# Kernel optimization log

Hardware: AMD Instinct MI355X
Metric: run time of the kernel (lower is better)

Reference implementation:

```python
import jax, jax.numpy as jnp
import numpy as np

B, D, H = 4096, 64, 1024  # batch, state dim, hidden width


def setup_inputs() -> dict:
    key = jax.random.key(0)
    ks = jax.random.split(key, 4)
    def w(k, shape, fan_in):
        return (jax.random.normal(k, shape, jnp.float32) / np.float32(np.sqrt(fan_in)))
    return {
        "x": jax.random.normal(ks[0], (B, 1 + D), jnp.float32),
        "W1": w(ks[1], (D, H), D),
        "b1": jnp.zeros((H,), jnp.float32),
        "W2": w(ks[2], (H, H), H),
        "b2": jnp.zeros((H,), jnp.float32),
        "W3": w(ks[3], (H, D), H),
        "b3": jnp.zeros((D,), jnp.float32),
    }


def _mlp(z, W1, b1, W2, b2, W3, b3):
    # tanh MLP vector field: d -> h -> h -> d
    h = jnp.tanh(z @ W1 + b1)
    h = jnp.tanh(h @ W2 + b2)
    return h @ W3 + b3


def reference(x, W1, b1, W2, b2, W3, b3):
    x_in = x[:, 1:]                        # [B, D] state (col 0 is logp channel)
    f = lambda z: _mlp(z, W1, b1, W2, b2, W3, b3)
    x_out = f(x_in)                        # [B, D]

    # Exact Jacobian trace: same math as the torch per-dim autograd.grad loop,
    # expressed as D forward-mode JVPs vmapped over the identity basis.
    eye = jnp.eye(x_in.shape[1], dtype=x.dtype)

    def diag_entry(e):                     # e: [D] basis vector
        _, t = jax.jvp(f, (x_in,), (jnp.broadcast_to(e, x_in.shape),))
        return t @ e                       # [B] = J[:, i, i]

    trJ = jnp.sum(jax.vmap(diag_entry)(eye), axis=0)  # [B]

    out = jnp.concatenate([-trJ[:, None], x_out], axis=1)  # [B, 1+D]
    return out + 0.0 * x  # faithful to `+ 0 * x` in the original
```

## Files before the change

kernel.cpp:

```cpp
#include <hip/hip_runtime.h>
#include <cmath>

typedef unsigned short u16;
typedef __attribute__((ext_vector_type(8))) short s8v;
typedef __attribute__((ext_vector_type(4))) float f4v;
typedef __attribute__((ext_vector_type(16))) float f16v;

__device__ __forceinline__ u16 f2bf(float f) {
    union { float f; unsigned u; } v; v.f = f;
    unsigned r = v.u + 0x7FFFu + ((v.u >> 16) & 1u);
    return (u16)(r >> 16);
}
__device__ __forceinline__ float tanh_fast(float x) {
    float e = __builtin_amdgcn_exp2f(x * 2.88539008177792681f);
    return 1.f - 2.f * __builtin_amdgcn_rcpf(1.f + e);
}
__device__ __forceinline__ int wslot(int row, int c) {
    return ((((c >> 2) << 6) | ((c & 3) << 4) | (row & 15)) ^ c);
}
__device__ __forceinline__ size_t fragoff(int n, int k) {
    return (((size_t)(n >> 5) * 64 + (k >> 4)) * 64 + (n & 31) + (((k >> 3) & 1) << 5)) * 8 + (k & 7);
}
__device__ __forceinline__ void gload_lds16(const u16* g, u16* l) {
    __builtin_amdgcn_global_load_lds(
        (const __attribute__((address_space(1))) void*)g,
        (__attribute__((address_space(3))) void*)l,
        16, 0, 0);
}

__launch_bounds__(256)
__global__ void cnf_prep(const float* __restrict__ x, const float* __restrict__ W1,
                         const float* __restrict__ W2, const float* __restrict__ W3,
                         u16* __restrict__ W2Tf, u16* __restrict__ VTf,
                         u16* __restrict__ xb, u16* __restrict__ W1T,
                         u16* __restrict__ W3Tf, float* __restrict__ trJ)
{
    __shared__ float w2s[32][33];
    __shared__ __align__(16) float w1s[64][36];
    const int a = blockIdx.x * 32;
    const int b = blockIdx.y * 32;
    const int t = threadIdx.x;

    #pragma unroll
    for (int it = 0; it < 4; ++it) {
        int idx = t + it * 256;
        w2s[idx >> 5][idx & 31] = W2[(a + (idx >> 5)) * 1024 + b + (idx & 31)];
    }
    #pragma unroll
    for (int it = 0; it < 8; ++it) {
        int idx = t + it * 256;
        w1s[idx >> 5][idx & 31] = W1[(idx >> 5) * 1024 + a + (idx & 31)];
    }
    __syncthreads();

    #pragma unroll
    for (int it = 0; it < 4; ++it) {
        int idx = t + it * 256;
        int rr = idx >> 5, cc = idx & 31;
        W2Tf[fragoff(b + rr, a + cc)] = f2bf(w2s[cc][rr]);
    }
    {
        const int q = t >> 3, pg = t & 7;
        const float* w3row = W3 + (b + q) * 64;
        f4v u = f4v{0.f, 0.f, 0.f, 0.f};
        #pragma unroll
        for (int i4 = 0; i4 < 16; ++i4) {
            f4v w3v = *(const f4v*)&w3row[i4 * 4];
            #pragma unroll
            for (int s = 0; s < 4; ++s) {
                f4v wv = *(const f4v*)&w1s[i4 * 4 + s][pg * 4];
                u += w3v[s] * wv;
            }
        }
        #pragma unroll
        for (int j = 0; j < 4; ++j) {
            const int pp = pg * 4 + j;
            VTf[fragoff(b + q, a + pp)] = f2bf(w2s[pp][q] * u[j]);
        }
    }
    {
        int bid = blockIdx.y * 32 + blockIdx.x;
        int e = bid * 256 + t;
        xb[e] = f2bf(x[(e >> 6) * 65 + 1 + (e & 63)]);
    }
    if (blockIdx.y == 0) {
        int pp = t >> 3, i0 = (t & 7) * 8;
        s8v v;
        #pragma unroll
        for (int j = 0; j < 8; ++j) v[j] = (short)f2bf(w1s[i0 + j][pp]);
        *(s8v*)&W1T[(a + pp) * 64 + i0] = v;
        if (t < 128) trJ[blockIdx.x * 128 + t] = 0.f;
    }
    if (blockIdx.y == 1) {
        int idx = blockIdx.x * 256 + t;
        int n = idx & 63, k0 = (idx >> 6) * 8;
        s8v v;
        #pragma unroll
        for (int j = 0; j < 8; ++j) v[j] = (short)f2bf(W3[(k0 + j) * 64 + n]);
        *(s8v*)&W3Tf[fragoff(n, k0)] = v;
    }
}

__launch_bounds__(256)
__global__ void cnf_gemm1(const u16* __restrict__ xb, const u16* __restrict__ W1T,
                          const float* __restrict__ b1,
                          u16* __restrict__ h1f, u16* __restrict__ g1f)
{
    __shared__ __align__(16) u16 lds[12 * 1024];
    __shared__ __align__(16) u16 hls[128 * 64];
    __shared__ __align__(16) u16 gls[128 * 64];
    const int t = threadIdx.x;
    const int wave = t >> 6, lane = t & 63;
    const int wm = wave >> 1, wn = wave & 1;
    const int g = lane >> 4, lr = lane & 15;
    const int arow0 = blockIdx.x * 128, bcol0 = blockIdx.y * 64;

    #pragma unroll
    for (int i = 0; i < 4; ++i) {
        int ch = t + i * 256, row = ch >> 3, c = ch & 7;
        *(s8v*)&lds[(row >> 4) * 1024 + wslot(row, c) * 8] =
            *(const s8v*)&xb[(arow0 + row) * 64 + c * 8];
    }
    #pragma unroll
    for (int i = 0; i < 2; ++i) {
        int ch = t + i * 256, row = ch >> 3, c = ch & 7;
        *(s8v*)&lds[(8 + (row >> 4)) * 1024 + wslot(row, c) * 8] =
            *(const s8v*)&W1T[(bcol0 + row) * 64 + c * 8];
    }
    __syncthreads();

    f4v acc[4][2];
    #pragma unroll
    for (int mi = 0; mi < 4; ++mi)
        #pragma unroll
        for (int ni = 0; ni < 2; ++ni) acc[mi][ni] = f4v{0.f,0.f,0.f,0.f};

    #pragma unroll
    for (int ks = 0; ks < 2; ++ks) {
        const int lo = (ks * 64 + (lane ^ ((ks * 4 + g) & 7))) * 8;
        s8v af[4], bf[2];
        #pragma unroll
        for (int mi = 0; mi < 4; ++mi) af[mi] = *(const s8v*)&lds[(wm * 4 + mi) * 1024 + lo];
        #pragma unroll
        for (int ni = 0; ni < 2; ++ni) bf[ni] = *(const s8v*)&lds[(8 + wn * 2 + ni) * 1024 + lo];
        #pragma unroll
        for (int mi = 0; mi < 4; ++mi)
            #pragma unroll
            for (int ni = 0; ni < 2; ++ni)
                acc[mi][ni] = __builtin_amdgcn_mfma_f32_16x16x32_bf16(af[mi], bf[ni], acc[mi][ni], 0, 0, 0);
    }

    #pragma unroll
    for (int mi = 0; mi < 4; ++mi) {
        const int rowl = wm * 64 + mi * 16 + g * 4;
        #pragma unroll
        for (int ni = 0; ni < 2; ++ni) {
            const int coll = wn * 32 + ni * 16 + lr;
            const float bv = b1[bcol0 + coll];
            const int cc = coll >> 3, jj = coll & 7;
            #pragma unroll
            for (int r = 0; r < 4; ++r) {
                const int row = rowl + r;
                float h = tanh_fast(acc[mi][ni][r] + bv);
                int idx = row * 64 + ((cc ^ (row & 7)) << 3) + jj;
                hls[idx] = f2bf(h);
                gls[idx] = f2bf(1.f - h * h);
            }
        }
    }
    __syncthreads();

    const int rt0 = arow0 >> 5, kk0 = bcol0 >> 4;
    #pragma unroll
    for (int i = 0; i < 4; ++i) {
        const int tile = (i * 256 + t) >> 6;
        const int ln = t & 63;
        const int rt = tile >> 2, kk = tile & 3;
        const int row = rt * 32 + (ln & 31);
        const int kb = kk * 16 + (ln >> 5) * 8;
        const int src = row * 64 + (((kb >> 3) ^ (row & 7)) << 3);
        const size_t dst = ((size_t)(rt0 + rt) * 64 + (kk0 + kk)) * 512 + ln * 8;
        *(s8v*)&h1f[dst] = *(const s8v*)&hls[src];
        *(s8v*)&g1f[dst] = *(const s8v*)&gls[src];
    }
}

#define STAGEA(kt, bb)                                                         \
    do { const int _kkg = (kt) * 2 + kwh;                                      \
         gload_lds16(h1f + ((size_t)rtg * 64 + _kkg) * 512 + lane * 8,         \
                     &lds[bb][wave * 512]);                                    \
         gload_lds16(g1f + ((size_t)rtg * 64 + _kkg) * 512 + lane * 8,         \
                     &lds[bb][4096 + wave * 512]);                             \
    } while (0)

#define LOADB(B, kkg)                                                          \
    do { _Pragma("unroll")                                                     \
         for (int _ks = 0; _ks < 2; ++_ks) {                                   \
             size_t _o = (((size_t)(ntb + wn) * 64 + (kkg) * 2 + _ks) * 64 + lane) * 8; \
             B[_ks*2 + 0] = *(const s8v*)&W2Tf[_o];                            \
             B[_ks*2 + 1] = *(const s8v*)&VTf[_o];                             \
         } } while (0)

#define MIDBODY(kt, Bc, Bn)                                                    \
    {                                                                          \
        if ((kt) < 31) { STAGEA((kt) + 1, ((kt) + 1) & 1); LOADB(Bn, (kt) + 1); } \
        const u16* buf = &lds[(kt) & 1][0];                                    \
        _Pragma("unroll")                                                      \
        for (int ks = 0; ks < 2; ++ks) {                                       \
            s8v a1[2], a2[2];                                                  \
            _Pragma("unroll")                                                  \
            for (int mt = 0; mt < 2; ++mt) {                                   \
                const int f = ((wrt * 2 + mt) * 2 + ks) * 512 + lane * 8;      \
                a1[mt] = *(const s8v*)&buf[f];                                 \
                a2[mt] = *(const s8v*)&buf[4096 + f];                          \
            }                                                                  \
            _Pragma("unroll")                                                  \
            for (int mt = 0; mt < 2; ++mt) {                                   \
                acc1[mt] = __builtin_amdgcn_mfma_f32_32x32x16_bf16(a1[mt], Bc[ks*2+0], acc1[mt], 0, 0, 0); \
                acc2[mt] = __builtin_amdgcn_mfma_f32_32x32x16_bf16(a2[mt], Bc[ks*2+1], acc2[mt], 0, 0, 0); \
            }                                                                  \
        }                                                                      \
        __syncthreads();                                                       \
    }

__launch_bounds__(512, 1)
__global__ void cnf_mid(const u16* __restrict__ h1f, const u16* __restrict__ g1f,
                        const u16* __restrict__ W2Tf, const u16* __restrict__ VTf,
                        const float* __restrict__ b2,
                        u16* __restrict__ h2f, float* __restrict__ trJ)
{
    __shared__ __align__(16) u16 lds[2][8192];

    const int t = threadIdx.x;
    const int wave = t >> 6, lane = t & 63;
    const int wrt = wave & 1;
    const int wn  = wave >> 1;
    const int bid = blockIdx.x;
    const int bx  = bid >> 3;
    const int by  = bid & 7;
    const int arow0 = bx * 128;
    const int ntb = by * 4;
    const int rtg = bx * 4 + (wave >> 1);
    const int kwh = wave & 1;

    f16v acc1[2], acc2[2];
    #pragma unroll
    for (int mt = 0; mt < 2; ++mt)
        #pragma unroll
        for (int r = 0; r < 16; ++r) { acc1[mt][r] = 0.f; acc2[mt][r] = 0.f; }

    s8v bA[4], bB[4];

    STAGEA(0, 0);
    LOADB(bA, 0);
    __syncthreads();

    for (int kt2 = 0; kt2 < 16; ++kt2) {
        const int kt = kt2 * 2;
        MIDBODY(kt,     bA, bB);
        MIDBODY(kt + 1, bB, bA);
    }

    const int l31 = lane & 31, lh = lane >> 5;
    #pragma unroll
    for (int mt = 0; mt < 2; ++mt) {
        const int rt = (arow0 >> 5) + wrt * 2 + mt;
        const int q0 = (ntb + wn) * 32;
        const float bv = b2[q0 + l31];
        const size_t hb = (((size_t)rt * 64 + ((q0 + l31) >> 4)) * 64
                           + (((l31 >> 3) & 1) << 5)) * 8 + (l31 & 7) + lh * 32;
        float tr[16];
        #pragma unroll
        for (int r = 0; r < 16; ++r) {
            float hh = tanh_fast(acc1[mt][r] + bv);
            float gg = 1.f - hh * hh;
            h2f[hb + ((r & 3) + ((r >> 2) << 3)) * 8] = f2bf(hh);
            tr[r] = acc2[mt][r] * gg;
        }
        #pragma unroll
        for (int off = 1; off < 32; off <<= 1)
            #pragma unroll
            for (int r = 0; r < 16; ++r) tr[r] += __shfl_xor(tr[r], off);
        if (l31 == 0) {
            const int rowb = arow0 + (wrt * 2 + mt) * 32 + lh * 4;
            #pragma unroll
            for (int r = 0; r < 16; ++r)
                atomicAdd(&trJ[rowb + (r & 3) + ((r >> 2) << 3)], tr[r]);
        }
    }
}

__launch_bounds__(256)
__global__ void cnf_out(const u16* __restrict__ h2f, const u16* __restrict__ W3Tf,
                        const float* __restrict__ b3, const float* __restrict__ trJ,
                        float* __restrict__ out)
{
    __shared__ float red[4][32][32];
    const int t = threadIdx.x;
    const int wave = t >> 6, lane = t & 63;
    const int rt = blockIdx.x;
    const int nb = blockIdx.y;

    f16v acc;
    #pragma unroll
    for (int r = 0; r < 16; ++r) acc[r] = 0.f;

    #pragma unroll
    for (int kki = 0; kki < 16; ++kki) {
        const int kk = wave * 16 + kki;
        s8v af = *(const s8v*)&h2f[(((size_t)rt * 64 + kk) * 64 + lane) * 8];
        s8v bf = *(const s8v*)&W3Tf[(((size_t)nb * 64 + kk) * 64 + lane) * 8];
        acc = __builtin_amdgcn_mfma_f32_32x32x16_bf16(af, bf, acc, 0, 0, 0);
    }
    const int l31 = lane & 31, lh = lane >> 5;
    #pragma unroll
    for (int r = 0; r < 16; ++r)
        red[wave][(r & 3) + ((r >> 2) << 3) + lh * 4][l31] = acc[r];
    __syncthreads();

    #pragma unroll
    for (int i = 0; i < 4; ++i) {
        int o = t + i * 256;
        int row = o >> 5, col = o & 31;
        float s = red[0][row][col] + red[1][row][col] + red[2][row][col]
                + red[3][row][col] + b3[nb * 32 + col];
        out[(size_t)(rt * 32 + row) * 65 + 1 + nb * 32 + col] = s;
    }
    if (nb == 0 && t < 32) out[(size_t)(rt * 32 + t) * 65] = -trJ[rt * 32 + t];
}

extern "C" void kernel_launch(void* const* d_in, const int* in_sizes, int n_in,
                              void* d_out, int out_size, void* d_ws, size_t ws_size,
                              hipStream_t stream) {
    const float* x  = (const float*)d_in[0];
    const float* W1 = (const float*)d_in[1];
    const float* b1 = (const float*)d_in[2];
    const float* W2 = (const float*)d_in[3];
    const float* b2 = (const float*)d_in[4];
    const float* W3 = (const float*)d_in[5];
    const float* b3 = (const float*)d_in[6];
    float* out = (float*)d_out;

    char* ws = (char*)d_ws;
    u16*   h1f = (u16*)(ws);
    u16*   g1f = (u16*)(ws + (size_t)( 8u << 20));
    u16*   h2f = (u16*)(ws + (size_t)(16u << 20));
    u16*   W2T = (u16*)(ws + (size_t)(24u << 20));
    u16*   VTb = (u16*)(ws + (size_t)(26u << 20));
    float* trJ = (float*)(ws + (size_t)(28u << 20));
    u16*   xbb = (u16*)(ws + (size_t)(28u << 20) + 65536);
    u16*   W1T = (u16*)(ws + (size_t)(28u << 20) + 65536 + 524288);
    u16*   W3T = (u16*)(ws + (size_t)(28u << 20) + 65536 + 524288 + 131072);

    cnf_prep <<<dim3(32, 32), 256, 0, stream>>>(x, W1, W2, W3, W2T, VTb, xbb, W1T, W3T, trJ);
    cnf_gemm1<<<dim3(32, 16), 256, 0, stream>>>(xbb, W1T, b1, h1f, g1f);
    cnf_mid  <<<256,          512, 0, stream>>>(h1f, g1f, W2T, VTb, b2, h2f, trJ);
    cnf_out  <<<dim3(128, 2), 256, 0, stream>>>(h2f, W3T, b3, trJ, out);
}
```

Before: 69.16 us.

## Replace direct global-to-LDS loads with register-staged prefetch and wider K phases

The mid GEMM kernel drops the global_load_lds staging in favour of loading A tiles (h1 and g1) into registers two phases ahead and writing them into LDS one phase ahead. Each phase now covers 64 of K instead of 32, which halves the number of barriers, and the LDS buffers are doubled in size. The full __syncthreads is replaced by an lgkmcnt wait followed by s_barrier, so outstanding global loads no longer have to drain at each barrier. In exchange the kernel uses more VGPRs for the staging registers and doubled B fragments, and a larger LDS footprint.

```diff
diff --git a/kernel.cpp b/kernel.cpp
--- a/kernel.cpp
+++ b/kernel.cpp
@@ -20,12 +20,6 @@
 }
 __device__ __forceinline__ size_t fragoff(int n, int k) {
     return (((size_t)(n >> 5) * 64 + (k >> 4)) * 64 + (n & 31) + (((k >> 3) & 1) << 5)) * 8 + (k & 7);
-}
-__device__ __forceinline__ void gload_lds16(const u16* g, u16* l) {
-    __builtin_amdgcn_global_load_lds(
-        (const __attribute__((address_space(1))) void*)g,
-        (__attribute__((address_space(3))) void*)l,
-        16, 0, 0);
 }
 
 __launch_bounds__(256)
@@ -185,34 +179,38 @@
     }
 }
 
-#define STAGEA(kt, bb)                                                         \
-    do { const int _kkg = (kt) * 2 + kwh;                                      \
-         gload_lds16(h1f + ((size_t)rtg * 64 + _kkg) * 512 + lane * 8,         \
-                     &lds[bb][wave * 512]);                                    \
-         gload_lds16(g1f + ((size_t)rtg * 64 + _kkg) * 512 + lane * 8,         \
-                     &lds[bb][4096 + wave * 512]);                             \
-    } while (0)
-
-#define LOADB(B, kkg)                                                          \
+#define LOADB(B, pp)                                                           \
     do { _Pragma("unroll")                                                     \
-         for (int _ks = 0; _ks < 2; ++_ks) {                                   \
-             size_t _o = (((size_t)(ntb + wn) * 64 + (kkg) * 2 + _ks) * 64 + lane) * 8; \
+         for (int _ks = 0; _ks < 4; ++_ks) {                                   \
+             size_t _o = (((size_t)(ntb + wn) * 64 + (pp) * 4 + _ks) * 64 + lane) * 8; \
              B[_ks*2 + 0] = *(const s8v*)&W2Tf[_o];                            \
              B[_ks*2 + 1] = *(const s8v*)&VTf[_o];                             \
          } } while (0)
 
-#define MIDBODY(kt, Bc, Bn)                                                    \
+#define PHASE(p, AwH, AwG, AlH, AlG, Bc, Bn)                                   \
     {                                                                          \
-        if ((kt) < 31) { STAGEA((kt) + 1, ((kt) + 1) & 1); LOADB(Bn, (kt) + 1); } \
-        const u16* buf = &lds[(kt) & 1][0];                                    \
+        if ((p) < 14) {                                                        \
+            const size_t _go = (size_t)((p) + 2) * 2048;                       \
+            AlH[0] = *(const s8v*)(h1f + sgo0 + _go);                          \
+            AlH[1] = *(const s8v*)(h1f + sgo1 + _go);                          \
+            AlG[0] = *(const s8v*)(g1f + sgo0 + _go);                          \
+            AlG[1] = *(const s8v*)(g1f + sgo1 + _go);                          \
+        }                                                                      \
+        if ((p) < 15) {                                                        \
+            u16* _wb = &lds[((p) + 1) & 1][0];                                 \
+            *(s8v*)&_wb[sdo0] = AwH[0];        *(s8v*)&_wb[sdo1] = AwH[1];     \
+            *(s8v*)&_wb[8192 + sdo0] = AwG[0]; *(s8v*)&_wb[8192 + sdo1] = AwG[1]; \
+            LOADB(Bn, (p) + 1);                                                \
+        }                                                                      \
+        const u16* _buf = &lds[(p) & 1][0];                                    \
         _Pragma("unroll")                                                      \
-        for (int ks = 0; ks < 2; ++ks) {                                       \
+        for (int ks = 0; ks < 4; ++ks) {                                       \
             s8v a1[2], a2[2];                                                  \
             _Pragma("unroll")                                                  \
             for (int mt = 0; mt < 2; ++mt) {                                   \
-                const int f = ((wrt * 2 + mt) * 2 + ks) * 512 + lane * 8;      \
-                a1[mt] = *(const s8v*)&buf[f];                                 \
-                a2[mt] = *(const s8v*)&buf[4096 + f];                          \
+                const int f = ((wrt * 2 + mt) * 4 + ks) * 512 + lane * 8;      \
+                a1[mt] = *(const s8v*)&_buf[f];                                \
+                a2[mt] = *(const s8v*)&_buf[8192 + f];                         \
             }                                                                  \
             _Pragma("unroll")                                                  \
             for (int mt = 0; mt < 2; ++mt) {                                   \
@@ -220,7 +218,10 @@
                 acc2[mt] = __builtin_amdgcn_mfma_f32_32x32x16_bf16(a2[mt], Bc[ks*2+1], acc2[mt], 0, 0, 0); \
             }                                                                  \
         }                                                                      \
-        __syncthreads();                                                       \
+        if ((p) < 15) {                                                        \
+            asm volatile("s_waitcnt lgkmcnt(0)" ::: "memory");                 \
+            __builtin_amdgcn_s_barrier();                                      \
+        }                                                                      \
     }
 
 __launch_bounds__(512, 1)
@@ -229,7 +230,7 @@
                         const float* __restrict__ b2,
                         u16* __restrict__ h2f, float* __restrict__ trJ)
 {
-    __shared__ __align__(16) u16 lds[2][8192];
+    __shared__ __align__(16) u16 lds[2][16384];
 
     const int t = threadIdx.x;
     const int wave = t >> 6, lane = t & 63;
@@ -240,8 +241,13 @@
     const int by  = bid & 7;
     const int arow0 = bx * 128;
     const int ntb = by * 4;
-    const int rtg = bx * 4 + (wave >> 1);
-    const int kwh = wave & 1;
+
+    const int lc8 = (t & 63) * 8;
+    const int rt0s = t >> 8, kkgs = (t >> 6) & 3;
+    const size_t sgo0 = ((size_t)(bx * 4 + rt0s) * 64 + kkgs) * 512 + lc8;
+    const size_t sgo1 = ((size_t)(bx * 4 + 2 + rt0s) * 64 + kkgs) * 512 + lc8;
+    const int sdo0 = (rt0s * 4 + kkgs) * 512 + lc8;
+    const int sdo1 = ((2 + rt0s) * 4 + kkgs) * 512 + lc8;
 
     f16v acc1[2], acc2[2];
     #pragma unroll
@@ -249,16 +255,26 @@
         #pragma unroll
         for (int r = 0; r < 16; ++r) { acc1[mt][r] = 0.f; acc2[mt][r] = 0.f; }
 
-    s8v bA[4], bB[4];
-
-    STAGEA(0, 0);
+    s8v raH[2], raG[2], rbH[2], rbG[2];
+    s8v bA[8], bB[8];
+
+    raH[0] = *(const s8v*)(h1f + sgo0); raH[1] = *(const s8v*)(h1f + sgo1);
+    raG[0] = *(const s8v*)(g1f + sgo0); raG[1] = *(const s8v*)(g1f + sgo1);
+    {
+        u16* wb = &lds[0][0];
+        *(s8v*)&wb[sdo0] = raH[0];        *(s8v*)&wb[sdo1] = raH[1];
+        *(s8v*)&wb[8192 + sdo0] = raG[0]; *(s8v*)&wb[8192 + sdo1] = raG[1];
+    }
+    raH[0] = *(const s8v*)(h1f + sgo0 + 2048); raH[1] = *(const s8v*)(h1f + sgo1 + 2048);
+    raG[0] = *(const s8v*)(g1f + sgo0 + 2048); raG[1] = *(const s8v*)(g1f + sgo1 + 2048);
     LOADB(bA, 0);
-    __syncthreads();
-
-    for (int kt2 = 0; kt2 < 16; ++kt2) {
-        const int kt = kt2 * 2;
-        MIDBODY(kt,     bA, bB);
-        MIDBODY(kt + 1, bB, bA);
+    asm volatile("s_waitcnt lgkmcnt(0)" ::: "memory");
+    __builtin_amdgcn_s_barrier();
+
+    for (int p2 = 0; p2 < 8; ++p2) {
+        const int p = p2 * 2;
+        PHASE(p,     raH, raG, rbH, rbG, bA, bB);
+        PHASE(p + 1, rbH, rbG, raH, raG, bB, bA);
     }
 
     const int l31 = lane & 31, lh = lane >> 5;
```

Measured after the change: 58.03 us. -16.1%, faster.

## Stage mid-GEMM A tiles via registers and shrink blocks to 256 threads

Applied to the files above, without the earlier changes.

Replaces the global_load_lds direct-to-LDS staging of the h1/g1 A tiles with register prefetching two k-steps ahead, followed by explicit LDS stores into the next buffer. The mid kernel is relaunched as a 32x16 grid of 256-thread blocks, each covering two N tiles instead of four. This gives 512 smaller blocks in place of 256 large ones. The aim is better occupancy and load overlap, at the cost of more registers, more B-operand reloads per block, and extra VGPR traffic for staging.

```diff
diff --git a/kernel.cpp b/kernel.cpp
--- a/kernel.cpp
+++ b/kernel.cpp
@@ -20,12 +20,6 @@
 }
 __device__ __forceinline__ size_t fragoff(int n, int k) {
     return (((size_t)(n >> 5) * 64 + (k >> 4)) * 64 + (n & 31) + (((k >> 3) & 1) << 5)) * 8 + (k & 7);
-}
-__device__ __forceinline__ void gload_lds16(const u16* g, u16* l) {
-    __builtin_amdgcn_global_load_lds(
-        (const __attribute__((address_space(1))) void*)g,
-        (__attribute__((address_space(3))) void*)l,
-        16, 0, 0);
 }
 
 __launch_bounds__(256)
@@ -185,45 +179,50 @@
     }
 }
 
-#define STAGEA(kt, bb)                                                         \
-    do { const int _kkg = (kt) * 2 + kwh;                                      \
-         gload_lds16(h1f + ((size_t)rtg * 64 + _kkg) * 512 + lane * 8,         \
-                     &lds[bb][wave * 512]);                                    \
-         gload_lds16(g1f + ((size_t)rtg * 64 + _kkg) * 512 + lane * 8,         \
-                     &lds[bb][4096 + wave * 512]);                             \
-    } while (0)
-
-#define LOADB(B, kkg)                                                          \
+#define LOADB(B, kt)                                                           \
     do { _Pragma("unroll")                                                     \
          for (int _ks = 0; _ks < 2; ++_ks) {                                   \
-             size_t _o = (((size_t)(ntb + wn) * 64 + (kkg) * 2 + _ks) * 64 + lane) * 8; \
+             size_t _o = (((size_t)(ntb + wn) * 64 + (kt) * 2 + _ks) * 512) + lane * 8; \
              B[_ks*2 + 0] = *(const s8v*)&W2Tf[_o];                            \
              B[_ks*2 + 1] = *(const s8v*)&VTf[_o];                             \
          } } while (0)
 
-#define MIDBODY(kt, Bc, Bn)                                                    \
+#define MIDBODY(kt, AwH, AwG, AlH, AlG, Bc, Bn)                                \
     {                                                                          \
-        if ((kt) < 31) { STAGEA((kt) + 1, ((kt) + 1) & 1); LOADB(Bn, (kt) + 1); } \
-        const u16* buf = &lds[(kt) & 1][0];                                    \
+        const u16* _buf = &lds[(kt) & 1][0];                                   \
+        s8v a1[2][2], a2[2][2];                                  \
         _Pragma("unroll")                                                      \
-        for (int ks = 0; ks < 2; ++ks) {                                       \
-            s8v a1[2], a2[2];                                                  \
+        for (int ks = 0; ks < 2; ++ks)                                         \
             _Pragma("unroll")                                                  \
             for (int mt = 0; mt < 2; ++mt) {                                   \
                 const int f = ((wrt * 2 + mt) * 2 + ks) * 512 + lane * 8;      \
-                a1[mt] = *(const s8v*)&buf[f];                                 \
-                a2[mt] = *(const s8v*)&buf[4096 + f];                          \
+                a1[ks][mt] = *(const s8v*)&_buf[f];                            \
+                a2[ks][mt] = *(const s8v*)&_buf[4096 + f];                     \
             }                                                                  \
+        if ((kt) < 30) {                                                       \
+            const size_t _go = (size_t)((kt) + 2) * 1024;                      \
+            AlH[0] = *(const s8v*)(h1f + sg0 + _go);                           \
+            AlH[1] = *(const s8v*)(h1f + sg1 + _go);                           \
+            AlG[0] = *(const s8v*)(g1f + sg0 + _go);                           \
+            AlG[1] = *(const s8v*)(g1f + sg1 + _go);                           \
+        }                                                                      \
+        if ((kt) < 31) {                                                       \
+            u16* _wb = &lds[((kt) + 1) & 1][0];                                \
+            *(s8v*)&_wb[sd0] = AwH[0];        *(s8v*)&_wb[sd1] = AwH[1];       \
+            *(s8v*)&_wb[4096 + sd0] = AwG[0]; *(s8v*)&_wb[4096 + sd1] = AwG[1];\
+            LOADB(Bn, (kt) + 1);                                               \
+        }                                                                      \
+        _Pragma("unroll")                                                      \
+        for (int ks = 0; ks < 2; ++ks)                                         \
             _Pragma("unroll")                                                  \
             for (int mt = 0; mt < 2; ++mt) {                                   \
-                acc1[mt] = __builtin_amdgcn_mfma_f32_32x32x16_bf16(a1[mt], Bc[ks*2+0], acc1[mt], 0, 0, 0); \
-                acc2[mt] = __builtin_amdgcn_mfma_f32_32x32x16_bf16(a2[mt], Bc[ks*2+1], acc2[mt], 0, 0, 0); \
+                acc1[mt] = __builtin_amdgcn_mfma_f32_32x32x16_bf16(a1[ks][mt], Bc[ks*2+0], acc1[mt], 0, 0, 0); \
+                acc2[mt] = __builtin_amdgcn_mfma_f32_32x32x16_bf16(a2[ks][mt], Bc[ks*2+1], acc2[mt], 0, 0, 0); \
             }                                                                  \
-        }                                                                      \
         __syncthreads();                                                       \
     }
 
-__launch_bounds__(512, 1)
+__launch_bounds__(256)
 __global__ void cnf_mid(const u16* __restrict__ h1f, const u16* __restrict__ g1f,
                         const u16* __restrict__ W2Tf, const u16* __restrict__ VTf,
                         const float* __restrict__ b2,
@@ -235,13 +234,17 @@
     const int wave = t >> 6, lane = t & 63;
     const int wrt = wave & 1;
     const int wn  = wave >> 1;
-    const int bid = blockIdx.x;
-    const int bx  = bid >> 3;
-    const int by  = bid & 7;
+    const int bx = blockIdx.x;
+    const int by = blockIdx.y;
     const int arow0 = bx * 128;
-    const int ntb = by * 4;
-    const int rtg = bx * 4 + (wave >> 1);
-    const int kwh = wave & 1;
+    const int ntb = by * 2;
+
+    const int lc8 = (t & 63) * 8;
+    const int c0rt = t >> 7, c0kk = (t >> 6) & 1;
+    const size_t sg0 = ((size_t)(bx * 4 + c0rt) * 64 + c0kk) * 512 + lc8;
+    const size_t sg1 = ((size_t)(bx * 4 + 2 + c0rt) * 64 + c0kk) * 512 + lc8;
+    const int sd0 = (c0rt * 2 + c0kk) * 512 + lc8;
+    const int sd1 = ((2 + c0rt) * 2 + c0kk) * 512 + lc8;
 
     f16v acc1[2], acc2[2];
     #pragma unroll
@@ -249,16 +252,25 @@
         #pragma unroll
         for (int r = 0; r < 16; ++r) { acc1[mt][r] = 0.f; acc2[mt][r] = 0.f; }
 
+    s8v raH[2], raG[2], rbH[2], rbG[2];
     s8v bA[4], bB[4];
 
-    STAGEA(0, 0);
+    raH[0] = *(const s8v*)(h1f + sg0); raH[1] = *(const s8v*)(h1f + sg1);
+    raG[0] = *(const s8v*)(g1f + sg0); raG[1] = *(const s8v*)(g1f + sg1);
+    {
+        u16* wb = &lds[0][0];
+        *(s8v*)&wb[sd0] = raH[0];        *(s8v*)&wb[sd1] = raH[1];
+        *(s8v*)&wb[4096 + sd0] = raG[0]; *(s8v*)&wb[4096 + sd1] = raG[1];
+    }
+    raH[0] = *(const s8v*)(h1f + sg0 + 1024); raH[1] = *(const s8v*)(h1f + sg1 + 1024);
+    raG[0] = *(const s8v*)(g1f + sg0 + 1024); raG[1] = *(const s8v*)(g1f + sg1 + 1024);
     LOADB(bA, 0);
     __syncthreads();
 
     for (int kt2 = 0; kt2 < 16; ++kt2) {
         const int kt = kt2 * 2;
-        MIDBODY(kt,     bA, bB);
-        MIDBODY(kt + 1, bB, bA);
+        MIDBODY(kt,     raH, raG, rbH, rbG, bA, bB);
+        MIDBODY(kt + 1, rbH, rbG, raH, raG, bB, bA);
     }
 
     const int l31 = lane & 31, lh = lane >> 5;
@@ -354,6 +366,6 @@
 
     cnf_prep <<<dim3(32, 32), 256, 0, stream>>>(x, W1, W2, W3, W2T, VTb, xbb, W1T, W3T, trJ);
     cnf_gemm1<<<dim3(32, 16), 256, 0, stream>>>(xbb, W1T, b1, h1f, g1f);
-    cnf_mid  <<<256,          512, 0, stream>>>(h1f, g1f, W2T, VTb, b2, h2f, trJ);
+    cnf_mid  <<<dim3(32, 16), 256, 0, stream>>>(h1f, g1f, W2T, VTb, b2, h2f, trJ);
     cnf_out  <<<dim3(128, 2), 256, 0, stream>>>(h2f, W3T, b3, trJ, out);
 }
```

New measurement: 56.19 us. -18.8%, faster.
